# Kernel tuning notes

Hardware: AMD Instinct MI355X
Metric: run time of the kernel (lower is better)

## Reference

```python
import jax, jax.numpy as jnp
import numpy as np

N_EMBD = 1024
HEAD_SIZE = 64
B, T = 8, 2048


def setup_inputs() -> dict:
    key = jax.random.key(0)
    k1, k2, k3, k4 = jax.random.split(key, 4)
    scale = 1.0 / np.sqrt(N_EMBD)
    return {
        "x": jax.random.normal(k1, (B, T, N_EMBD), dtype=jnp.float32),
        "Wq": jax.random.normal(k2, (N_EMBD, HEAD_SIZE), dtype=jnp.float32) * scale,
        "Wk": jax.random.normal(k3, (N_EMBD, HEAD_SIZE), dtype=jnp.float32) * scale,
        "Wv": jax.random.normal(k4, (N_EMBD, HEAD_SIZE), dtype=jnp.float32) * scale,
    }


def reference(x, Wq, Wk, Wv):
    # x: [B, T, C]; projections (no bias)
    q = jnp.einsum("btc,ch->bth", x, Wq)
    k = jnp.einsum("btc,ch->bth", x, Wk)
    v = jnp.einsum("btc,ch->bth", x, Wv)
    head_size = k.shape[-1]
    # scaled scores [B, T, T]
    wei = jnp.einsum("bth,bsh->bts", q, k) * (head_size ** -0.5)
    # causal mask (lower-triangular keeps)
    Tlen = x.shape[1]
    causal = jnp.tril(jnp.ones((Tlen, Tlen), dtype=bool))
    wei = jnp.where(causal[None, :, :], wei, -jnp.inf)
    wei = jax.nn.softmax(wei, axis=-1)
    # dropout p=0 (eval) -> identity
    out = jnp.einsum("bts,bsh->bth", wei, v)
    return out
```

## Files before the change

kernel.cpp:

```cpp
#include <hip/hip_runtime.h>
#include <hip/hip_bf16.h>
#include <math.h>

#define Bn 8
#define Tn 2048
#define Cn 1024
#define Hn 64

typedef __attribute__((ext_vector_type(8))) short short8;
typedef __attribute__((ext_vector_type(4))) float floatx4;

#define ATTN_SCALE 0.18033688011112042f

__device__ inline unsigned short f2bf(float f) {
    union { float f; unsigned int u; } x; x.f = f;
    unsigned int r = x.u + 0x7fffu + ((x.u >> 16) & 1u);
    return (unsigned short)(r >> 16);
}

__device__ inline uint2 pack4bf(float4 v) {
    __hip_bfloat162 lo = __float22bfloat162_rn(make_float2(v.x, v.y));
    __hip_bfloat162 hi = __float22bfloat162_rn(make_float2(v.z, v.w));
    uint2 r;
    r.x = *reinterpret_cast<unsigned int*>(&lo);
    r.y = *reinterpret_cast<unsigned int*>(&hi);
    return r;
}

__device__ inline float rsum16(float v) {
    v += __shfl_xor(v, 1);
    v += __shfl_xor(v, 2);
    v += __shfl_xor(v, 4);
    v += __shfl_xor(v, 8);
    return v;
}

__global__ __launch_bounds__(256) void prep_w(
    const float* __restrict__ Wq, const float* __restrict__ Wk,
    const float* __restrict__ Wv, unsigned short* __restrict__ Wfrag)
{
    const int gid = blockIdx.x * 256 + threadIdx.x;
    const int c    = gid >> 11;
    const int rem  = gid & 2047;
    const int ks   = rem >> 6;
    const int lane = rem & 63;
    const int ln = lane & 15, qd = lane >> 4;
    const int mat = c >> 2, nc = c & 3;
    const float* W = (mat == 0) ? Wq : (mat == 1) ? Wk : Wv;
    const float sc = (mat == 0) ? ATTN_SCALE : 1.0f;
    const int col = nc * 16 + ln;
    unsigned short o[8];
    #pragma unroll
    for (int j = 0; j < 8; ++j)
        o[j] = f2bf(W[(size_t)(ks * 32 + qd * 8 + j) * Hn + col] * sc);
    *reinterpret_cast<short8*>(Wfrag + (size_t)gid * 8) = *reinterpret_cast<short8*>(o);
}

__global__ __launch_bounds__(256, 4) void proj_mfma(
    const float* __restrict__ x, const unsigned short* __restrict__ Wfrag,
    unsigned short* __restrict__ qbf, unsigned short* __restrict__ kfrag,
    unsigned short* __restrict__ vfrag)
{
    __shared__ unsigned short xs[2][16][136];

    const int ln   = threadIdx.x & 15;
    const int quad = (threadIdx.x >> 4) & 3;
    const int w    = threadIdx.x >> 6;
    const int lane = threadIdx.x & 63;
    const int row0 = blockIdx.x * 16;

    const int srow = threadIdx.x >> 4;
    const int sf   = threadIdx.x & 15;
    const float4* xrow4 = reinterpret_cast<const float4*>(x + (size_t)(row0 + srow) * Cn);

    floatx4 acc[3];
    #pragma unroll
    for (int i = 0; i < 3; ++i) acc[i] = (floatx4){0.f, 0.f, 0.f, 0.f};

    float4 pa_ = xrow4[sf], pb_ = xrow4[sf + 16];
    *reinterpret_cast<uint2*>(&xs[0][srow][sf * 4])      = pack4bf(pa_);
    *reinterpret_cast<uint2*>(&xs[0][srow][sf * 4 + 64]) = pack4bf(pb_);
    pa_ = xrow4[32 + sf]; pb_ = xrow4[32 + sf + 16];

    for (int c = 0; c < 8; ++c) {
        __syncthreads();
        if (c < 7) {
            *reinterpret_cast<uint2*>(&xs[(c + 1) & 1][srow][sf * 4])      = pack4bf(pa_);
            *reinterpret_cast<uint2*>(&xs[(c + 1) & 1][srow][sf * 4 + 64]) = pack4bf(pb_);
        }
        if (c < 6) {
            pa_ = xrow4[(c + 2) * 32 + sf];
            pb_ = xrow4[(c + 2) * 32 + sf + 16];
        }
        #pragma unroll
        for (int kk = 0; kk < 4; ++kk) {
            const short8 a = *reinterpret_cast<const short8*>(
                &xs[c & 1][ln][kk * 32 + quad * 8]);
            #pragma unroll
            for (int i = 0; i < 3; ++i) {
                const int cc = w * 3 + i;
                const short8 b = *reinterpret_cast<const short8*>(
                    Wfrag + ((size_t)((cc * 32) + c * 4 + kk) * 64 + lane) * 8);
                acc[i] = __builtin_amdgcn_mfma_f32_16x16x32_bf16(a, b, acc[i], 0, 0, 0);
            }
        }
    }

    const int t0   = row0 + quad * 4;
    const int b    = t0 >> 11;
    const int tloc = t0 & 2047;
    #pragma unroll
    for (int i = 0; i < 3; ++i) {
        const int idx = w * 3 + i;
        const int mat = idx >> 2, ch = idx & 3;
        if (mat == 0) {
            #pragma unroll
            for (int r = 0; r < 4; ++r)
                qbf[(size_t)(t0 + r) * Hn + ch * 16 + ln] = f2bf(acc[i][r]);
        } else if (mat == 1) {
            const int kc = tloc >> 4;
            const int ks = ch >> 1;
            const int lq = (ch & 1) * 2 + (ln >> 3);
            #pragma unroll
            for (int r = 0; r < 4; ++r) {
                const int lanep = (quad * 4 + r) + 16 * lq;
                kfrag[(((size_t)(b * 128 + kc) * 2 + ks) * 64 + lanep) * 8 + (ln & 7)]
                    = f2bf(acc[i][r]);
            }
        } else {
            const int kb32 = tloc >> 5;
            const int off  = t0 & 31;
            const int qd   = off >> 3;
            const int j0   = off & 7;
            const int lanep = ln + 16 * qd;
            ushort4 pk;
            pk.x = f2bf(acc[i][0]); pk.y = f2bf(acc[i][1]);
            pk.z = f2bf(acc[i][2]); pk.w = f2bf(acc[i][3]);
            *reinterpret_cast<ushort4*>(
                vfrag + (((size_t)(b * 64 + kb32) * 4 + ch) * 64 + lanep) * 8 + j0) = pk;
        }
    }
}

__global__ __launch_bounds__(256, 4) void attn_mfma(
    const unsigned short* __restrict__ qbf, const unsigned short* __restrict__ kfrag,
    const unsigned short* __restrict__ vt, float* __restrict__ out)
{
    __shared__ unsigned short p_lds[4][16 * 40];
    __shared__ float o_lds[4][16][68];
    __shared__ float l_lds[4][16];

    const int j  = blockIdx.x;
    const int b  = j & 7;
    const int ti = 127 - (j >> 3);
    const int q0 = ti * 16;

    const int ln   = threadIdx.x & 15;
    const int quad = (threadIdx.x >> 4) & 3;
    const int w    = threadIdx.x >> 6;
    const int lane = threadIdx.x & 63;

    const unsigned short* qb = qbf + (size_t)b * Tn * Hn;
    const unsigned short* Kb = kfrag + (size_t)b * 131072;
    const unsigned short* Vb = vt + (size_t)b * 131072;

    const short8 aq0 = *reinterpret_cast<const short8*>(qb + (size_t)(q0 + ln) * Hn + quad * 8);
    const short8 aq1 = *reinterpret_cast<const short8*>(qb + (size_t)(q0 + ln) * Hn + 32 + quad * 8);

    floatx4 O[4];
    #pragma unroll
    for (int c = 0; c < 4; ++c) O[c] = (floatx4){0.f, 0.f, 0.f, 0.f};
    float lp[4] = {0.f, 0.f, 0.f, 0.f};

    const int ntiles = (q0 + 47) >> 5;
    const int per    = (ntiles + 3) >> 2;
    const int beg    = w * per;
    const int end    = min(beg + per, ntiles);
    unsigned short* pP = p_lds[w];

    short8 kf[4];
    if (beg < end) {
        #pragma unroll
        for (int u = 0; u < 4; ++u)
            kf[u] = *reinterpret_cast<const short8*>(Kb + ((size_t)(beg * 4 + u)) * 512 + lane * 8);
    }

    for (int t = beg; t < end; ++t) {
        const int tn = (t + 1 < end) ? (t + 1) : t;
        short8 kn[4], vf[4];
        #pragma unroll
        for (int u = 0; u < 4; ++u) {
            kn[u] = *reinterpret_cast<const short8*>(Kb + ((size_t)(tn * 4 + u)) * 512 + lane * 8);
            vf[u] = *reinterpret_cast<const short8*>(Vb + ((size_t)(t * 4 + u)) * 512 + lane * 8);
        }

        const floatx4 z = (floatx4){0.f, 0.f, 0.f, 0.f};
        floatx4 S[2];
        #pragma unroll
        for (int s = 0; s < 2; ++s) {
            S[s] = __builtin_amdgcn_mfma_f32_16x16x32_bf16(aq0, kf[s * 2], z, 0, 0, 0);
            S[s] = __builtin_amdgcn_mfma_f32_16x16x32_bf16(aq1, kf[s * 2 + 1], S[s], 0, 0, 0);
        }

        const bool diag = (t == ntiles - 1);
        #pragma unroll
        for (int s = 0; s < 2; ++s) {
            #pragma unroll
            for (int r = 0; r < 4; ++r) {
                float sv = S[s][r];
                if (diag && (t * 32 + s * 16 + ln > q0 + quad * 4 + r)) sv = -1e30f;
                const unsigned int pu = __float_as_uint(exp2f(sv));
                lp[r] += __uint_as_float(pu & 0xffff0000u);
                pP[(quad * 4 + r) * 40 + s * 16 + ln] = (unsigned short)(pu >> 16);
            }
        }
        __asm__ volatile("s_waitcnt lgkmcnt(0)" ::: "memory");
        const short8 pa = *reinterpret_cast<const short8*>(pP + ln * 40 + quad * 8);
        #pragma unroll
        for (int c = 0; c < 4; ++c)
            O[c] = __builtin_amdgcn_mfma_f32_16x16x32_bf16(pa, vf[c], O[c], 0, 0, 0);
        #pragma unroll
        for (int u = 0; u < 4; ++u) kf[u] = kn[u];
    }

    #pragma unroll
    for (int c = 0; c < 4; ++c)
        #pragma unroll
        for (int r = 0; r < 4; ++r)
            o_lds[w][quad * 4 + r][c * 16 + ln] = O[c][r];
    #pragma unroll
    for (int r = 0; r < 4; ++r) {
        const float ls = rsum16(lp[r]);
        if (ln == 0) l_lds[w][quad * 4 + r] = ls;
    }
    __syncthreads();

    const int qq = threadIdx.x >> 4;
    const int dg = threadIdx.x & 15;
    const float ltot = l_lds[0][qq] + l_lds[1][qq] + l_lds[2][qq] + l_lds[3][qq];
    const float inv = 1.0f / ltot;
    const float4 a0 = *reinterpret_cast<float4*>(&o_lds[0][qq][dg * 4]);
    const float4 a1 = *reinterpret_cast<float4*>(&o_lds[1][qq][dg * 4]);
    const float4 a2 = *reinterpret_cast<float4*>(&o_lds[2][qq][dg * 4]);
    const float4 a3 = *reinterpret_cast<float4*>(&o_lds[3][qq][dg * 4]);
    float4 r;
    r.x = (a0.x + a1.x + a2.x + a3.x) * inv;
    r.y = (a0.y + a1.y + a2.y + a3.y) * inv;
    r.z = (a0.z + a1.z + a2.z + a3.z) * inv;
    r.w = (a0.w + a1.w + a2.w + a3.w) * inv;
    *reinterpret_cast<float4*>(out + ((size_t)b * Tn + q0 + qq) * Hn + dg * 4) = r;
}

extern "C" void kernel_launch(void* const* d_in, const int* in_sizes, int n_in,
                              void* d_out, int out_size, void* d_ws, size_t ws_size,
                              hipStream_t stream) {
    (void)in_sizes; (void)n_in; (void)out_size; (void)ws_size;
    const float* x  = (const float*)d_in[0];
    const float* Wq = (const float*)d_in[1];
    const float* Wk = (const float*)d_in[2];
    const float* Wv = (const float*)d_in[3];
    float* out = (float*)d_out;

    unsigned short* Wfrag = (unsigned short*)d_ws;
    unsigned short* qbf   = Wfrag + (size_t)196608;
    unsigned short* kfr   = qbf + (size_t)Bn * Tn * Hn;
    unsigned short* vfr   = kfr + (size_t)Bn * 131072;

    prep_w<<<96, 256, 0, stream>>>(Wq, Wk, Wv, Wfrag);
    proj_mfma<<<(Bn * Tn) / 16, 256, 0, stream>>>(x, Wfrag, qbf, kfr, vfr);
    attn_mfma<<<Bn * (Tn / 16), 256, 0, stream>>>(qbf, kfr, vfr, out);
}
```

Baseline: 131.3 us.

## Split projection K across waves with direct global x loads and LDS reduction

Drops the shared-memory bf16 staging of x and double buffering in the projection kernel. Each wave now loads its x fragment straight from global memory, converts it to bf16 in registers, and covers half of the reduction dimension for six output column tiles. The two K-halves are then summed through LDS. This removes the per-chunk barriers and LDS round trips, but each x element is now loaded by several waves, loads use a strided per-lane pattern, and more accumulator registers are live.

Measured after the change: 143.8 us. +9.6%, slower.

```diff
diff --git a/kernel.cpp b/kernel.cpp
--- a/kernel.cpp
+++ b/kernel.cpp
@@ -61,57 +61,60 @@
     unsigned short* __restrict__ qbf, unsigned short* __restrict__ kfrag,
     unsigned short* __restrict__ vfrag)
 {
-    __shared__ unsigned short xs[2][16][136];
+    __shared__ float part[2][6][16][17];
 
     const int ln   = threadIdx.x & 15;
     const int quad = (threadIdx.x >> 4) & 3;
     const int w    = threadIdx.x >> 6;
     const int lane = threadIdx.x & 63;
+    const int wk = w & 1, wn = w >> 1;
     const int row0 = blockIdx.x * 16;
 
-    const int srow = threadIdx.x >> 4;
-    const int sf   = threadIdx.x & 15;
-    const float4* xrow4 = reinterpret_cast<const float4*>(x + (size_t)(row0 + srow) * Cn);
-
-    floatx4 acc[3];
-    #pragma unroll
-    for (int i = 0; i < 3; ++i) acc[i] = (floatx4){0.f, 0.f, 0.f, 0.f};
-
-    float4 pa_ = xrow4[sf], pb_ = xrow4[sf + 16];
-    *reinterpret_cast<uint2*>(&xs[0][srow][sf * 4])      = pack4bf(pa_);
-    *reinterpret_cast<uint2*>(&xs[0][srow][sf * 4 + 64]) = pack4bf(pb_);
-    pa_ = xrow4[32 + sf]; pb_ = xrow4[32 + sf + 16];
-
-    for (int c = 0; c < 8; ++c) {
-        __syncthreads();
-        if (c < 7) {
-            *reinterpret_cast<uint2*>(&xs[(c + 1) & 1][srow][sf * 4])      = pack4bf(pa_);
-            *reinterpret_cast<uint2*>(&xs[(c + 1) & 1][srow][sf * 4 + 64]) = pack4bf(pb_);
-        }
-        if (c < 6) {
-            pa_ = xrow4[(c + 2) * 32 + sf];
-            pb_ = xrow4[(c + 2) * 32 + sf + 16];
-        }
-        #pragma unroll
-        for (int kk = 0; kk < 4; ++kk) {
-            const short8 a = *reinterpret_cast<const short8*>(
-                &xs[c & 1][ln][kk * 32 + quad * 8]);
-            #pragma unroll
-            for (int i = 0; i < 3; ++i) {
-                const int cc = w * 3 + i;
-                const short8 b = *reinterpret_cast<const short8*>(
-                    Wfrag + ((size_t)((cc * 32) + c * 4 + kk) * 64 + lane) * 8);
-                acc[i] = __builtin_amdgcn_mfma_f32_16x16x32_bf16(a, b, acc[i], 0, 0, 0);
-            }
-        }
-    }
+    const float* xr = x + (size_t)(row0 + ln) * Cn + wk * 512 + quad * 8;
+
+    floatx4 acc[6];
+    #pragma unroll
+    for (int i = 0; i < 6; ++i) acc[i] = (floatx4){0.f, 0.f, 0.f, 0.f};
+
+    #pragma unroll 2
+    for (int ks = 0; ks < 16; ++ks) {
+        const float4 xa = *reinterpret_cast<const float4*>(xr + ks * 32);
+        const float4 xb = *reinterpret_cast<const float4*>(xr + ks * 32 + 4);
+        union { uint2 u2[2]; short8 s8; } a;
+        a.u2[0] = pack4bf(xa);
+        a.u2[1] = pack4bf(xb);
+        const int kstep = wk * 16 + ks;
+        #pragma unroll
+        for (int i = 0; i < 6; ++i) {
+            const int cc = wn * 6 + i;
+            const short8 b = *reinterpret_cast<const short8*>(
+                Wfrag + ((size_t)(cc * 32 + kstep) * 64 + lane) * 8);
+            acc[i] = __builtin_amdgcn_mfma_f32_16x16x32_bf16(a.s8, b, acc[i], 0, 0, 0);
+        }
+    }
+
+    if (wk == 1) {
+        #pragma unroll
+        for (int i = 0; i < 6; ++i)
+            #pragma unroll
+            for (int r = 0; r < 4; ++r)
+                part[wn][i][quad * 4 + r][ln] = acc[i][r];
+    }
+    __syncthreads();
+    if (wk == 1) return;
+
+    #pragma unroll
+    for (int i = 0; i < 6; ++i)
+        #pragma unroll
+        for (int r = 0; r < 4; ++r)
+            acc[i][r] += part[wn][i][quad * 4 + r][ln];
 
     const int t0   = row0 + quad * 4;
     const int b    = t0 >> 11;
     const int tloc = t0 & 2047;
     #pragma unroll
-    for (int i = 0; i < 3; ++i) {
-        const int idx = w * 3 + i;
+    for (int i = 0; i < 6; ++i) {
+        const int idx = wn * 6 + i;
         const int mat = idx >> 2, ch = idx & 3;
         if (mat == 0) {
             #pragma unroll
```

## Load full x tile into fragment-ordered LDS once, drop double-buffered loop

Applied to the files above, without the earlier changes.

The projection kernel now issues all 16 float4 global loads per thread up front and converts them to bf16. It stores the whole 16x1024 x tile into shared memory in MFMA fragment order, then runs 32 MFMA k-steps with a single barrier and conflict-free contiguous LDS reads. This removes the per-chunk syncthreads and the padded row layout of the double-buffered pipeline. The cost is 32KB of LDS per block and 64 extra registers for the staged loads, which can lower occupancy under launch_bounds(256,4). Global-load latency is also no longer overlapped with compute inside a block.

Result: faster. 125.0 us (-4.8%).

```diff
diff --git a/kernel.cpp b/kernel.cpp
--- a/kernel.cpp
+++ b/kernel.cpp
@@ -61,7 +61,7 @@
     unsigned short* __restrict__ qbf, unsigned short* __restrict__ kfrag,
     unsigned short* __restrict__ vfrag)
 {
-    __shared__ unsigned short xs[2][16][136];
+    __shared__ unsigned short xs[32 * 512];
 
     const int ln   = threadIdx.x & 15;
     const int quad = (threadIdx.x >> 4) & 3;
@@ -73,36 +73,33 @@
     const int sf   = threadIdx.x & 15;
     const float4* xrow4 = reinterpret_cast<const float4*>(x + (size_t)(row0 + srow) * Cn);
 
+    float4 ld[16];
+    #pragma unroll
+    for (int it = 0; it < 16; ++it)
+        ld[it] = xrow4[sf + 16 * it];
+    #pragma unroll
+    for (int it = 0; it < 16; ++it) {
+        const int f4g = sf + 16 * it;
+        const int s = f4g >> 3;
+        const int q = (f4g >> 1) & 3;
+        const int j = (f4g & 1) * 4;
+        *reinterpret_cast<uint2*>(&xs[s * 512 + (q * 16 + srow) * 8 + j]) = pack4bf(ld[it]);
+    }
+    __syncthreads();
+
     floatx4 acc[3];
     #pragma unroll
     for (int i = 0; i < 3; ++i) acc[i] = (floatx4){0.f, 0.f, 0.f, 0.f};
 
-    float4 pa_ = xrow4[sf], pb_ = xrow4[sf + 16];
-    *reinterpret_cast<uint2*>(&xs[0][srow][sf * 4])      = pack4bf(pa_);
-    *reinterpret_cast<uint2*>(&xs[0][srow][sf * 4 + 64]) = pack4bf(pb_);
-    pa_ = xrow4[32 + sf]; pb_ = xrow4[32 + sf + 16];
-
-    for (int c = 0; c < 8; ++c) {
-        __syncthreads();
-        if (c < 7) {
-            *reinterpret_cast<uint2*>(&xs[(c + 1) & 1][srow][sf * 4])      = pack4bf(pa_);
-            *reinterpret_cast<uint2*>(&xs[(c + 1) & 1][srow][sf * 4 + 64]) = pack4bf(pb_);
-        }
-        if (c < 6) {
-            pa_ = xrow4[(c + 2) * 32 + sf];
-            pb_ = xrow4[(c + 2) * 32 + sf + 16];
-        }
-        #pragma unroll
-        for (int kk = 0; kk < 4; ++kk) {
-            const short8 a = *reinterpret_cast<const short8*>(
-                &xs[c & 1][ln][kk * 32 + quad * 8]);
-            #pragma unroll
-            for (int i = 0; i < 3; ++i) {
-                const int cc = w * 3 + i;
-                const short8 b = *reinterpret_cast<const short8*>(
-                    Wfrag + ((size_t)((cc * 32) + c * 4 + kk) * 64 + lane) * 8);
-                acc[i] = __builtin_amdgcn_mfma_f32_16x16x32_bf16(a, b, acc[i], 0, 0, 0);
-            }
+    #pragma unroll 4
+    for (int s = 0; s < 32; ++s) {
+        const short8 a = *reinterpret_cast<const short8*>(&xs[s * 512 + lane * 8]);
+        #pragma unroll
+        for (int i = 0; i < 3; ++i) {
+            const int cc = w * 3 + i;
+            const short8 b = *reinterpret_cast<const short8*>(
+                Wfrag + ((size_t)(cc * 32 + s) * 64 + lane) * 8);
+            acc[i] = __builtin_amdgcn_mfma_f32_16x16x32_bf16(a, b, acc[i], 0, 0, 0);
         }
     }
 
```
